# Performance work log

Measured on AMD Instinct MI355X. Metric: run time of the kernel, lower is better.

The kernel has to match this reference:

```python
import jax, jax.numpy as jnp
import numpy as np

N = 100000      # nodes
E = 1600000     # edges per adjacency
NFEAT = 128
NH1 = 128
NH2 = 64
ND1 = 64
P = 100000      # link-prediction pairs


def setup_inputs() -> dict:
    key = jax.random.key(0)
    ks = jax.random.split(key, 20)

    def unif(k, shape, fan):
        s = 1.0 / np.sqrt(fan)
        return jax.random.uniform(k, shape, jnp.float32, -s, s)

    return {
        "x": jax.random.normal(ks[0], (N, NFEAT), jnp.float32),
        "o_edges": jax.random.randint(ks[1], (2, E), 0, N, jnp.int32),
        "o_vals": jax.random.uniform(ks[2], (E,), jnp.float32),
        "s_edges": jax.random.randint(ks[3], (2, E), 0, N, jnp.int32),
        "s_vals": jax.random.uniform(ks[4], (E,), jnp.float32),
        "idx": jax.random.randint(ks[5], (2, P), 0, N, jnp.int64),
        "W_o1": unif(ks[6], (NFEAT, NH1), NFEAT),
        "b_o1": unif(ks[7], (NH1,), NFEAT),
        "W_o2": unif(ks[8], (NH1, NH2), NH1),
        "b_o2": unif(ks[9], (NH2,), NH1),
        "W_s1": unif(ks[10], (NFEAT, NH1), NFEAT),
        "b_s1": unif(ks[11], (NH1,), NFEAT),
        "W_s2": unif(ks[12], (NH1, NH2), NH1),
        "b_s2": unif(ks[13], (NH2,), NH1),
        "ag1": unif(ks[14], (NH2,), NH2),
        "ag2": unif(ks[15], (NH2,), NH2),
        "dec1_W": unif(ks[16], (2 * NH2, ND1), 2 * NH2),
        "dec1_b": unif(ks[17], (ND1,), 2 * NH2),
        "dec2_W": unif(ks[18], (ND1, 1), ND1),
        "dec2_b": unif(ks[19], (1,), ND1),
    }


def _gcn(h, edges, vals, W, b):
    # GraphConvolution: support = h @ W; out = spmm(adj, support) + b
    support = h @ W                                # [N, d_out]
    msg = support[edges[1]] * vals[:, None]        # gather src rows, scale by edge weight
    agg = jax.ops.segment_sum(msg, edges[0], num_segments=N)
    return agg + b


def reference(x, o_edges, o_vals, s_edges, s_vals, idx,
              W_o1, b_o1, W_o2, b_o2, W_s1, b_s1, W_s2, b_s2,
              ag1, ag2, dec1_W, dec1_b, dec2_W, dec2_b):
    # branch 1 (original graph); dropout is identity in eval mode
    x1 = jax.nn.relu(_gcn(x, o_edges, o_vals, W_o1, b_o1))
    x1 = _gcn(x1, o_edges, o_vals, W_o2, b_o2)     # [N, NH2]
    # branch 2 (skip graph)
    x2 = jax.nn.relu(_gcn(x, s_edges, s_vals, W_s1, b_s1))
    x2 = _gcn(x2, s_edges, s_vals, W_s2, b_s2)     # [N, NH2]
    # attention gating: per-node scalar gate broadcast over features
    g = (x1 @ ag1)[:, None] * x1 + (x2 @ ag2)[:, None] * x2  # [N, NH2]
    # gather pair endpoints, concat, MLP decoder (no activation in between)
    feat = jnp.concatenate((g[idx[0]], g[idx[1]]), axis=1)   # [P, 2*NH2]
    o = feat @ dec1_W + dec1_b
    return o @ dec2_W + dec2_b                               # [P, 1]
```

## Files before the change

### kernel.cpp

```cpp
#include <hip/hip_runtime.h>


constexpr int BKT_SHIFT = 8;
constexpr int BKT_NODES = 256;
constexpr int SORT_CAP  = 7168;

typedef __attribute__((ext_vector_type(8))) short bf16x8;
typedef __attribute__((ext_vector_type(4))) float f32x4;

__device__ __forceinline__ float wave_sum64(float x) {
#pragma unroll
    for (int o = 32; o > 0; o >>= 1) x += __shfl_xor(x, o, 64);
    return x;
}

__device__ __forceinline__ unsigned short f2bf(float f) {
    unsigned int u = __float_as_uint(f);
    u += 0x7FFF + ((u >> 16) & 1);
    return (unsigned short)(u >> 16);
}

__device__ __forceinline__ float2 bf2f2(unsigned int u) {
    float2 r;
    r.x = __uint_as_float(u << 16);
    r.y = __uint_as_float(u & 0xFFFF0000u);
    return r;
}


__global__ __launch_bounds__(256) void bhist_k(const int* __restrict__ eo,
                                               const int* __restrict__ es,
                                               int* __restrict__ bcnt,
                                               int E, int N, int nb) {
    __shared__ int lh[1024];
    for (int i = threadIdx.x; i < nb; i += 256) lh[i] = 0;
    __syncthreads();
    int total = 2 * E;
    for (int t = blockIdx.x * 256 + threadIdx.x; t < total; t += gridDim.x * 256) {
        int g = (t >= E) ? 1 : 0;
        int e = g ? t - E : t;
        int dst = (g ? es : eo)[e];
        atomicAdd(&lh[(g * N + dst) >> BKT_SHIFT], 1);
    }
    __syncthreads();
    for (int i = threadIdx.x; i < nb; i += 256) {
        int v = lh[i];
        if (v) atomicAdd(&bcnt[i], v);
    }
}

__global__ __launch_bounds__(1024) void bscan_k(const int* __restrict__ bcnt,
                                                int* __restrict__ bbase,
                                                int* __restrict__ bcur,
                                                int nb, int total) {
    __shared__ int sh[1024];
    int t = threadIdx.x;
    int v = (t < nb) ? bcnt[t] : 0;
    sh[t] = v;
    __syncthreads();
#pragma unroll
    for (int o = 1; o < 1024; o <<= 1) {
        int tv = (t >= o) ? sh[t - o] : 0;
        __syncthreads();
        sh[t] += tv;
        __syncthreads();
    }
    if (t < nb) {
        int b = sh[t] - v;
        bbase[t] = b;
        bcur[t] = b;
    }
    if (t == 0) bbase[nb] = total;
}

__global__ __launch_bounds__(256) void bin_k(const int* __restrict__ eo,
                                             const float* __restrict__ vo,
                                             const int* __restrict__ es,
                                             const float* __restrict__ vs,
                                             int* __restrict__ bcur,
                                             int2* __restrict__ binned,
                                             int E, int N, int nb, int chunk) {
    __shared__ int lcnt[1024];
    __shared__ int lbase[1024];
    int c0 = blockIdx.x * chunk;
    int c1 = min(c0 + chunk, 2 * E);
    for (int i = threadIdx.x; i < nb; i += 256) lcnt[i] = 0;
    __syncthreads();
    for (int t = c0 + threadIdx.x; t < c1; t += 256) {
        int g = (t >= E) ? 1 : 0;
        int e = g ? t - E : t;
        int dst = (g ? es : eo)[e];
        atomicAdd(&lcnt[(g * N + dst) >> BKT_SHIFT], 1);
    }
    __syncthreads();
    for (int i = threadIdx.x; i < nb; i += 256) {
        int v = lcnt[i];
        lbase[i] = v ? atomicAdd(&bcur[i], v) : 0;
        lcnt[i] = 0;
    }
    __syncthreads();
    for (int t = c0 + threadIdx.x; t < c1; t += 256) {
        int g = (t >= E) ? 1 : 0;
        int e = g ? t - E : t;
        const int* edges = g ? es : eo;
        int dst = edges[e];
        int dc = g * N + dst;
        int b = dc >> BKT_SHIFT;
        int pos = lbase[b] + atomicAdd(&lcnt[b], 1);
        int src = edges[E + e];
        float val = (g ? vs : vo)[e];
        binned[pos] = make_int2(((dc & (BKT_NODES - 1)) << 17) | src,
                                __float_as_int(val));
    }
}

__global__ __launch_bounds__(256) void sort_k(const int* __restrict__ bbase,
                                              const int2* __restrict__ binned,
                                              int2* __restrict__ csr,
                                              int* __restrict__ rp2,
                                              int n2, int total) {
    __shared__ int2 lrec[SORT_CAP];
    __shared__ int ldeg[BKT_NODES];
    __shared__ int lsc[BKT_NODES];
    int b = blockIdx.x;
    int base = bbase[b];
    int count = min(bbase[b + 1] - base, SORT_CAP);
    int tid = threadIdx.x;
    for (int k = tid; k < count; k += 256) lrec[k] = binned[base + k];
    ldeg[tid] = 0;
    __syncthreads();
    for (int k = tid; k < count; k += 256) atomicAdd(&ldeg[lrec[k].x >> 17], 1);
    __syncthreads();
    int v = ldeg[tid];
    lsc[tid] = v;
    __syncthreads();
#pragma unroll
    for (int o = 1; o < 256; o <<= 1) {
        int tv = (tid >= o) ? lsc[tid - o] : 0;
        __syncthreads();
        lsc[tid] += tv;
        __syncthreads();
    }
    int excl = lsc[tid] - v;
    int node = b * BKT_NODES + tid;
    if (node < n2) rp2[node] = base + excl;
    if (b == 0 && tid == 0) rp2[n2] = total;
    ldeg[tid] = excl;
    __syncthreads();
    for (int k = tid; k < count; k += 256) {
        int2 r = lrec[k];
        int dl = r.x >> 17;
        int p = atomicAdd(&ldeg[dl], 1);
        csr[base + p] = make_int2(r.x & 0x1FFFF, r.y);
    }
}

__global__ void prep_k(const float* __restrict__ dec1_W, const float* __restrict__ dec1_b,
                       const float* __restrict__ dec2_W, const float* __restrict__ dec2_b,
                       const float* __restrict__ W_o2, const float* __restrict__ b_o2,
                       const float* __restrict__ W_s2, const float* __restrict__ b_s2,
                       const float* __restrict__ ag1, const float* __restrict__ ag2,
                       float* __restrict__ Mo, float* __restrict__ Ms,
                       float* __restrict__ beta, float* __restrict__ cc) {
    __shared__ float vsh[128];
    int t = threadIdx.x;
    float s = 0.f;
    for (int j = 0; j < 64; ++j) s += dec1_W[t * 64 + j] * dec2_W[j];
    vsh[t] = s;
    __syncthreads();
    const float* vlo = vsh;
    const float* vhi = vsh + 64;
    float m0 = 0, m1 = 0, m2 = 0, n0 = 0, n1 = 0, n2 = 0;
    for (int k = 0; k < 64; ++k) {
        float wo = W_o2[t * 64 + k], wsv = W_s2[t * 64 + k];
        m0 += wo * ag1[k];  m1 += wo * vlo[k];  m2 += wo * vhi[k];
        n0 += wsv * ag2[k]; n1 += wsv * vlo[k]; n2 += wsv * vhi[k];
    }
    Mo[0 * 128 + t] = m0; Mo[1 * 128 + t] = m1; Mo[2 * 128 + t] = m2;
    Ms[0 * 128 + t] = n0; Ms[1 * 128 + t] = n1; Ms[2 * 128 + t] = n2;
    if (t == 0) {
        float b0 = 0, b1 = 0, b2 = 0, s0 = 0, s1 = 0, s2 = 0, c0 = 0;
        for (int k = 0; k < 64; ++k) {
            b0 += b_o2[k] * ag1[k]; b1 += b_o2[k] * vlo[k]; b2 += b_o2[k] * vhi[k];
            s0 += b_s2[k] * ag2[k]; s1 += b_s2[k] * vlo[k]; s2 += b_s2[k] * vhi[k];
            c0 += dec1_b[k] * dec2_W[k];
        }
        beta[0] = b0; beta[1] = b1; beta[2] = b2;
        beta[4] = s0; beta[5] = s1; beta[6] = s2;
        *cc = c0 + dec2_b[0];
    }
}

__global__ __launch_bounds__(256) void gemm_mfma2_k(const float* __restrict__ X,
                                                    const float* __restrict__ W0,
                                                    const float* __restrict__ W1,
                                                    unsigned short* __restrict__ S0,
                                                    unsigned short* __restrict__ S1,
                                                    int nrows) {
    __shared__ unsigned short XL[128 * 128];
    __shared__ unsigned short WT[128 * 128];

    const int tid = threadIdx.x;
    const int row0 = blockIdx.x * 128;
    const float4* X4 = (const float4*)X;

#pragma unroll
    for (int i = 0; i < 16; ++i) {
        int f = i * 256 + tid;
        int r = f >> 5, q = f & 31;
        int gr = row0 + r;
        if (gr >= nrows) gr = nrows - 1;
        float4 v = X4[(size_t)gr * 32 + q];
        unsigned int w0 = (unsigned int)f2bf(v.x) | ((unsigned int)f2bf(v.y) << 16);
        unsigned int w1 = (unsigned int)f2bf(v.z) | ((unsigned int)f2bf(v.w) << 16);
        int bp = (q >> 1) ^ (r & 15);
        unsigned int* p = (unsigned int*)&XL[r * 128 + bp * 8 + (q & 1) * 4];
        p[0] = w0;
        p[1] = w1;
    }

    const int w4 = (tid >> 6) * 32;
    const int lr = tid & 15;
    const int kg = (tid >> 4) & 3;

    bf16x8 a[2][4];
    bool a_loaded = false;

    for (int br = 0; br < 2; ++br) {
        const float* W = br ? W1 : W0;
        unsigned short* S = br ? S1 : S0;
        if (br) __syncthreads();
        {
            int c = tid >> 1;
            int kh = (tid & 1) * 64;
#pragma unroll 8
            for (int k2 = 0; k2 < 32; ++k2) {
                int k = kh + 2 * k2;
                unsigned int lo = f2bf(W[k * 128 + c]);
                unsigned int hi = f2bf(W[(k + 1) * 128 + c]);
                int bp = (k >> 3) ^ (c & 15);
                ((unsigned int*)&WT[c * 128 + bp * 8])[(k >> 1) & 3] = lo | (hi << 16);
            }
        }
        __syncthreads();

        if (!a_loaded) {
            a_loaded = true;
#pragma unroll
            for (int rt = 0; rt < 2; ++rt)
#pragma unroll
                for (int kt = 0; kt < 4; ++kt)
                    a[rt][kt] = *(const bf16x8*)&XL[(w4 + rt * 16 + lr) * 128 +
                                                    (((kt * 4 + kg) ^ lr) * 8)];
        }

        f32x4 acc[2][8];
#pragma unroll
        for (int rt = 0; rt < 2; ++rt)
#pragma unroll
            for (int ct = 0; ct < 8; ++ct) acc[rt][ct] = (f32x4){0.f, 0.f, 0.f, 0.f};

#pragma unroll
        for (int ct = 0; ct < 8; ++ct) {
#pragma unroll
            for (int kt = 0; kt < 4; ++kt) {
                bf16x8 b = *(const bf16x8*)&WT[(ct * 16 + lr) * 128 +
                                               (((kt * 4 + kg) ^ lr) * 8)];
                acc[0][ct] = __builtin_amdgcn_mfma_f32_16x16x32_bf16(a[0][kt], b, acc[0][ct], 0, 0, 0);
                acc[1][ct] = __builtin_amdgcn_mfma_f32_16x16x32_bf16(a[1][kt], b, acc[1][ct], 0, 0, 0);
            }
        }

#pragma unroll
        for (int rt = 0; rt < 2; ++rt)
#pragma unroll
            for (int j = 0; j < 4; ++j) {
                int gr = row0 + w4 + rt * 16 + kg * 4 + j;
                if (gr < nrows) {
                    size_t rb = (size_t)gr * 128 + lr;
#pragma unroll
                    for (int ct = 0; ct < 8; ++ct)
                        S[rb + ct * 16] = f2bf(acc[rt][ct][j]);
                }
            }
    }
}

__global__ __launch_bounds__(256) void seg_spmm_fused2_k(
    const int* __restrict__ rp2, const int2* __restrict__ csr,
    const unsigned short* __restrict__ So, const unsigned short* __restrict__ Ss,
    const float* __restrict__ bias_o, const float* __restrict__ bias_s,
    const float* __restrict__ Mo, const float* __restrict__ Ms,
    float4* __restrict__ To, float4* __restrict__ Ts, int n) {
    const int* rp;
    const unsigned int* S;
    const float* bias;
    const float* M;
    float4* T;
    if (blockIdx.y == 0) {
        rp = rp2;     S = (const unsigned int*)So; bias = bias_o; M = Mo; T = To;
    } else {
        rp = rp2 + n; S = (const unsigned int*)Ss; bias = bias_s; M = Ms; T = Ts;
    }
    int wid = (blockIdx.x * 256 + threadIdx.x) >> 6;
    int lane = threadIdx.x & 63;
    if (wid >= n) return;
    int e = rp[wid], end = rp[wid + 1];
    float ax = 0.f, ay = 0.f;
    for (; e + 7 < end; e += 8) {
        int2 c0 = csr[e],     c1 = csr[e + 1], c2 = csr[e + 2], c3 = csr[e + 3];
        int2 c4 = csr[e + 4], c5 = csr[e + 5], c6 = csr[e + 6], c7 = csr[e + 7];
        float2 m0 = bf2f2(S[c0.x * 64 + lane]);
        float2 m1 = bf2f2(S[c1.x * 64 + lane]);
        float2 m2 = bf2f2(S[c2.x * 64 + lane]);
        float2 m3 = bf2f2(S[c3.x * 64 + lane]);
        float2 m4 = bf2f2(S[c4.x * 64 + lane]);
        float2 m5 = bf2f2(S[c5.x * 64 + lane]);
        float2 m6 = bf2f2(S[c6.x * 64 + lane]);
        float2 m7 = bf2f2(S[c7.x * 64 + lane]);
        float v0 = __int_as_float(c0.y), v1 = __int_as_float(c1.y);
        float v2 = __int_as_float(c2.y), v3 = __int_as_float(c3.y);
        float v4 = __int_as_float(c4.y), v5 = __int_as_float(c5.y);
        float v6 = __int_as_float(c6.y), v7 = __int_as_float(c7.y);
        ax += m0.x * v0 + m1.x * v1 + m2.x * v2 + m3.x * v3;
        ay += m0.y * v0 + m1.y * v1 + m2.y * v2 + m3.y * v3;
        ax += m4.x * v4 + m5.x * v5 + m6.x * v6 + m7.x * v7;
        ay += m4.y * v4 + m5.y * v5 + m6.y * v6 + m7.y * v7;
    }
    for (; e + 3 < end; e += 4) {
        int2 c0 = csr[e], c1 = csr[e + 1], c2 = csr[e + 2], c3 = csr[e + 3];
        float2 m0 = bf2f2(S[c0.x * 64 + lane]);
        float2 m1 = bf2f2(S[c1.x * 64 + lane]);
        float2 m2 = bf2f2(S[c2.x * 64 + lane]);
        float2 m3 = bf2f2(S[c3.x * 64 + lane]);
        float v0 = __int_as_float(c0.y), v1 = __int_as_float(c1.y);
        float v2 = __int_as_float(c2.y), v3 = __int_as_float(c3.y);
        ax += m0.x * v0 + m1.x * v1 + m2.x * v2 + m3.x * v3;
        ay += m0.y * v0 + m1.y * v1 + m2.y * v2 + m3.y * v3;
    }
    for (; e < end; ++e) {
        int2 c = csr[e];
        float2 m = bf2f2(S[c.x * 64 + lane]);
        float v = __int_as_float(c.y);
        ax += m.x * v;
        ay += m.y * v;
    }
    float2 bb = ((const float2*)bias)[lane];
    ax = fmaxf(ax + bb.x, 0.f);
    ay = fmaxf(ay + bb.y, 0.f);
    float2 M0 = ((const float2*)(M + 0 * 128))[lane];
    float2 M1 = ((const float2*)(M + 1 * 128))[lane];
    float2 M2 = ((const float2*)(M + 2 * 128))[lane];
    float d = wave_sum64(ax * M0.x + ay * M0.y);
    float u = wave_sum64(ax * M1.x + ay * M1.y);
    float w = wave_sum64(ax * M2.x + ay * M2.y);
    if (lane == 0) T[wid] = make_float4(d, u, w, 0.f);
}

__global__ __launch_bounds__(256) void gate_k(
    const int* __restrict__ rp2, const int2* __restrict__ csr,
    const float4* __restrict__ To, const float4* __restrict__ Ts,
    const float* __restrict__ beta,
    float* __restrict__ a, float* __restrict__ b, int n) {
    int i = blockIdx.x * 256 + threadIdx.x;
    if (i >= n) return;
    float d1 = 0.f, u1 = 0.f, w1 = 0.f;
    {
        int e = rp2[i], end = rp2[i + 1];
        for (; e + 3 < end; e += 4) {
            int2 c0 = csr[e], c1 = csr[e + 1], c2 = csr[e + 2], c3 = csr[e + 3];
            float4 t0 = To[c0.x];
            float4 t1 = To[c1.x];
            float4 t2 = To[c2.x];
            float4 t3 = To[c3.x];
            float v0 = __int_as_float(c0.y), v1 = __int_as_float(c1.y);
            float v2 = __int_as_float(c2.y), v3 = __int_as_float(c3.y);
            d1 += t0.x * v0 + t1.x * v1 + t2.x * v2 + t3.x * v3;
            u1 += t0.y * v0 + t1.y * v1 + t2.y * v2 + t3.y * v3;
            w1 += t0.z * v0 + t1.z * v1 + t2.z * v2 + t3.z * v3;
        }
        for (; e < end; ++e) {
            int2 c = csr[e];
            float4 t = To[c.x];
            float v = __int_as_float(c.y);
            d1 += t.x * v; u1 += t.y * v; w1 += t.z * v;
        }
    }
    float d2 = 0.f, u2 = 0.f, w2 = 0.f;
    {
        int e = rp2[n + i], end = rp2[n + i + 1];
        for (; e + 3 < end; e += 4) {
            int2 c0 = csr[e], c1 = csr[e + 1], c2 = csr[e + 2], c3 = csr[e + 3];
            float4 t0 = Ts[c0.x];
            float4 t1 = Ts[c1.x];
            float4 t2 = Ts[c2.x];
            float4 t3 = Ts[c3.x];
            float v0 = __int_as_float(c0.y), v1 = __int_as_float(c1.y);
            float v2 = __int_as_float(c2.y), v3 = __int_as_float(c3.y);
            d2 += t0.x * v0 + t1.x * v1 + t2.x * v2 + t3.x * v3;
            u2 += t0.y * v0 + t1.y * v1 + t2.y * v2 + t3.y * v3;
            w2 += t0.z * v0 + t1.z * v1 + t2.z * v2 + t3.z * v3;
        }
        for (; e < end; ++e) {
            int2 c = csr[e];
            float4 t = Ts[c.x];
            float v = __int_as_float(c.y);
            d2 += t.x * v; u2 += t.y * v; w2 += t.z * v;
        }
    }
    d1 += beta[0]; u1 += beta[1]; w1 += beta[2];
    d2 += beta[4]; u2 += beta[5]; w2 += beta[6];
    a[i] = d1 * u1 + d2 * u2;
    b[i] = d1 * w1 + d2 * w2;
}

__global__ __launch_bounds__(256) void decode_k(const int* __restrict__ idx,
                                                const float* __restrict__ a,
                                                const float* __restrict__ b,
                                                const float* __restrict__ c,
                                                float* __restrict__ out, int P) {
    int i = blockIdx.x * 256 + threadIdx.x;
    if (i >= P) return;
    out[i] = a[idx[i]] + b[idx[P + i]] + *c;
}


extern "C" void kernel_launch(void* const* d_in, const int* in_sizes, int n_in,
                              void* d_out, int out_size, void* d_ws, size_t ws_size,
                              hipStream_t stream) {
    const float* x      = (const float*)d_in[0];
    const int*   o_edges= (const int*)d_in[1];
    const float* o_vals = (const float*)d_in[2];
    const int*   s_edges= (const int*)d_in[3];
    const float* s_vals = (const float*)d_in[4];
    const int*   idx    = (const int*)d_in[5];
    const float* W_o1   = (const float*)d_in[6];
    const float* b_o1   = (const float*)d_in[7];
    const float* W_o2   = (const float*)d_in[8];
    const float* b_o2   = (const float*)d_in[9];
    const float* W_s1   = (const float*)d_in[10];
    const float* b_s1   = (const float*)d_in[11];
    const float* W_s2   = (const float*)d_in[12];
    const float* b_s2   = (const float*)d_in[13];
    const float* ag1    = (const float*)d_in[14];
    const float* ag2    = (const float*)d_in[15];
    const float* dec1_W = (const float*)d_in[16];
    const float* dec1_b = (const float*)d_in[17];
    const float* dec2_W = (const float*)d_in[18];
    const float* dec2_b = (const float*)d_in[19];
    float* out = (float*)d_out;

    const int N = in_sizes[0] / 128;
    const int E = in_sizes[1] / 2;
    const int P = out_size;
    const int n2 = 2 * N;
    const int nb = (n2 + BKT_NODES - 1) / BKT_NODES;

    const size_t NBH = (size_t)N * 128 * 2;

    char* ws = (char*)d_ws;
    size_t off = 0;
    auto alloc = [&](size_t bytes) {
        char* p = ws + off;
        off += (bytes + 255) & ~(size_t)255;
        return p;
    };

    unsigned short* B0 = (unsigned short*)alloc(NBH);
    unsigned short* B1 = (unsigned short*)alloc(NBH);
    float4* To = (float4*)alloc((size_t)N * 16);
    float4* Ts = (float4*)alloc((size_t)N * 16);
    float* av = (float*)alloc((size_t)P * 4);
    float* bv = (float*)alloc((size_t)P * 4);
    float* Mo = (float*)alloc(3 * 128 * 4);
    float* Ms = (float*)alloc(3 * 128 * 4);
    float* beta = (float*)alloc(32);
    float* cc = (float*)alloc(16);
    int* bcnt  = (int*)alloc((size_t)nb * 4);
    int* bbase = (int*)alloc((size_t)(nb + 1) * 4);
    int* bcur  = (int*)alloc((size_t)nb * 4);
    int* rp2   = (int*)alloc((size_t)(n2 + 1) * 4);
    int2* binned = (int2*)alloc((size_t)2 * E * 8);
    int2* csr    = (int2*)alloc((size_t)2 * E * 8);

    const int nblk = (N + 255) / 256;

    hipMemsetAsync(bcnt, 0, (size_t)nb * 4, stream);
    bhist_k<<<512, 256, 0, stream>>>(o_edges, s_edges, bcnt, E, N, nb);
    bscan_k<<<1, 1024, 0, stream>>>(bcnt, bbase, bcur, nb, 2 * E);
    const int chunk = 8192;
    bin_k<<<(2 * E + chunk - 1) / chunk, 256, 0, stream>>>(
        o_edges, o_vals, s_edges, s_vals, bcur, binned, E, N, nb, chunk);
    sort_k<<<nb, 256, 0, stream>>>(bbase, binned, csr, rp2, n2, 2 * E);

    prep_k<<<1, 128, 0, stream>>>(dec1_W, dec1_b, dec2_W, dec2_b,
                                  W_o2, b_o2, W_s2, b_s2, ag1, ag2,
                                  Mo, Ms, beta, cc);

    gemm_mfma2_k<<<(N + 127) / 128, 256, 0, stream>>>(x, W_o1, W_s1, B0, B1, N);

    dim3 sgrid((N * 64 + 255) / 256, 2);
    seg_spmm_fused2_k<<<sgrid, 256, 0, stream>>>(rp2, csr, B0, B1, b_o1, b_s1,
                                                 Mo, Ms, To, Ts, N);

    gate_k<<<nblk, 256, 0, stream>>>(rp2, csr, To, Ts, beta, av, bv, N);

    decode_k<<<(P + 255) / 256, 256, 0, stream>>>(idx, av, bv, cc, out, P);
}
```

Baseline: 313.5 us.

## Merge GEMM, edge binning and prep into one role-dispatched kernel

Combines the dense feature GEMM, the edge-binning pass and the tiny weight-prep kernel into a single launch where each block picks a role by block index. The independent GEMM and binning work can then run concurrently on the GPU instead of serialising across separate launches, and two launch boundaries go away. In exchange, every block reserves 64 KB of shared memory, including the binning and prep blocks that need far less, which may reduce occupancy for those roles.

New measurement: 293.7 us (median of 2 runs). 1.07x faster.

```diff
diff --git a/kernel.cpp b/kernel.cpp
--- a/kernel.cpp
+++ b/kernel.cpp
@@ -73,16 +73,18 @@
     if (t == 0) bbase[nb] = total;
 }
 
-__global__ __launch_bounds__(256) void bin_k(const int* __restrict__ eo,
-                                             const float* __restrict__ vo,
-                                             const int* __restrict__ es,
-                                             const float* __restrict__ vs,
-                                             int* __restrict__ bcur,
-                                             int2* __restrict__ binned,
-                                             int E, int N, int nb, int chunk) {
-    __shared__ int lcnt[1024];
-    __shared__ int lbase[1024];
-    int c0 = blockIdx.x * chunk;
+
+__device__ __forceinline__ void bin_role(unsigned char* smem, int bb,
+                                         const int* __restrict__ eo,
+                                         const float* __restrict__ vo,
+                                         const int* __restrict__ es,
+                                         const float* __restrict__ vs,
+                                         int* __restrict__ bcur,
+                                         int2* __restrict__ binned,
+                                         int E, int N, int nb, int chunk) {
+    int* lcnt = (int*)smem;
+    int* lbase = lcnt + 1024;
+    int c0 = bb * chunk;
     int c1 = min(c0 + chunk, 2 * E);
     for (int i = threadIdx.x; i < nb; i += 256) lcnt[i] = 0;
     __syncthreads();
@@ -114,94 +116,18 @@
     }
 }
 
-__global__ __launch_bounds__(256) void sort_k(const int* __restrict__ bbase,
-                                              const int2* __restrict__ binned,
-                                              int2* __restrict__ csr,
-                                              int* __restrict__ rp2,
-                                              int n2, int total) {
-    __shared__ int2 lrec[SORT_CAP];
-    __shared__ int ldeg[BKT_NODES];
-    __shared__ int lsc[BKT_NODES];
-    int b = blockIdx.x;
-    int base = bbase[b];
-    int count = min(bbase[b + 1] - base, SORT_CAP);
-    int tid = threadIdx.x;
-    for (int k = tid; k < count; k += 256) lrec[k] = binned[base + k];
-    ldeg[tid] = 0;
-    __syncthreads();
-    for (int k = tid; k < count; k += 256) atomicAdd(&ldeg[lrec[k].x >> 17], 1);
-    __syncthreads();
-    int v = ldeg[tid];
-    lsc[tid] = v;
-    __syncthreads();
-#pragma unroll
-    for (int o = 1; o < 256; o <<= 1) {
-        int tv = (tid >= o) ? lsc[tid - o] : 0;
-        __syncthreads();
-        lsc[tid] += tv;
-        __syncthreads();
-    }
-    int excl = lsc[tid] - v;
-    int node = b * BKT_NODES + tid;
-    if (node < n2) rp2[node] = base + excl;
-    if (b == 0 && tid == 0) rp2[n2] = total;
-    ldeg[tid] = excl;
-    __syncthreads();
-    for (int k = tid; k < count; k += 256) {
-        int2 r = lrec[k];
-        int dl = r.x >> 17;
-        int p = atomicAdd(&ldeg[dl], 1);
-        csr[base + p] = make_int2(r.x & 0x1FFFF, r.y);
-    }
-}
-
-__global__ void prep_k(const float* __restrict__ dec1_W, const float* __restrict__ dec1_b,
-                       const float* __restrict__ dec2_W, const float* __restrict__ dec2_b,
-                       const float* __restrict__ W_o2, const float* __restrict__ b_o2,
-                       const float* __restrict__ W_s2, const float* __restrict__ b_s2,
-                       const float* __restrict__ ag1, const float* __restrict__ ag2,
-                       float* __restrict__ Mo, float* __restrict__ Ms,
-                       float* __restrict__ beta, float* __restrict__ cc) {
-    __shared__ float vsh[128];
-    int t = threadIdx.x;
-    float s = 0.f;
-    for (int j = 0; j < 64; ++j) s += dec1_W[t * 64 + j] * dec2_W[j];
-    vsh[t] = s;
-    __syncthreads();
-    const float* vlo = vsh;
-    const float* vhi = vsh + 64;
-    float m0 = 0, m1 = 0, m2 = 0, n0 = 0, n1 = 0, n2 = 0;
-    for (int k = 0; k < 64; ++k) {
-        float wo = W_o2[t * 64 + k], wsv = W_s2[t * 64 + k];
-        m0 += wo * ag1[k];  m1 += wo * vlo[k];  m2 += wo * vhi[k];
-        n0 += wsv * ag2[k]; n1 += wsv * vlo[k]; n2 += wsv * vhi[k];
-    }
-    Mo[0 * 128 + t] = m0; Mo[1 * 128 + t] = m1; Mo[2 * 128 + t] = m2;
-    Ms[0 * 128 + t] = n0; Ms[1 * 128 + t] = n1; Ms[2 * 128 + t] = n2;
-    if (t == 0) {
-        float b0 = 0, b1 = 0, b2 = 0, s0 = 0, s1 = 0, s2 = 0, c0 = 0;
-        for (int k = 0; k < 64; ++k) {
-            b0 += b_o2[k] * ag1[k]; b1 += b_o2[k] * vlo[k]; b2 += b_o2[k] * vhi[k];
-            s0 += b_s2[k] * ag2[k]; s1 += b_s2[k] * vlo[k]; s2 += b_s2[k] * vhi[k];
-            c0 += dec1_b[k] * dec2_W[k];
-        }
-        beta[0] = b0; beta[1] = b1; beta[2] = b2;
-        beta[4] = s0; beta[5] = s1; beta[6] = s2;
-        *cc = c0 + dec2_b[0];
-    }
-}
-
-__global__ __launch_bounds__(256) void gemm_mfma2_k(const float* __restrict__ X,
-                                                    const float* __restrict__ W0,
-                                                    const float* __restrict__ W1,
-                                                    unsigned short* __restrict__ S0,
-                                                    unsigned short* __restrict__ S1,
-                                                    int nrows) {
-    __shared__ unsigned short XL[128 * 128];
-    __shared__ unsigned short WT[128 * 128];
+__device__ __forceinline__ void gemm_role(unsigned char* smem, int blk,
+                                          const float* __restrict__ X,
+                                          const float* __restrict__ W0,
+                                          const float* __restrict__ W1,
+                                          unsigned short* __restrict__ S0,
+                                          unsigned short* __restrict__ S1,
+                                          int nrows) {
+    unsigned short* XL = (unsigned short*)smem;
+    unsigned short* WT = XL + 128 * 128;
 
     const int tid = threadIdx.x;
-    const int row0 = blockIdx.x * 128;
+    const int row0 = blk * 128;
     const float4* X4 = (const float4*)X;
 
 #pragma unroll
@@ -283,6 +209,124 @@
                         S[rb + ct * 16] = f2bf(acc[rt][ct][j]);
                 }
             }
+    }
+}
+
+__device__ __forceinline__ void prep_role(unsigned char* smem,
+                                          const float* __restrict__ dec1_W,
+                                          const float* __restrict__ dec1_b,
+                                          const float* __restrict__ dec2_W,
+                                          const float* __restrict__ dec2_b,
+                                          const float* __restrict__ W_o2,
+                                          const float* __restrict__ b_o2,
+                                          const float* __restrict__ W_s2,
+                                          const float* __restrict__ b_s2,
+                                          const float* __restrict__ ag1,
+                                          const float* __restrict__ ag2,
+                                          float* __restrict__ Mo,
+                                          float* __restrict__ Ms,
+                                          float* __restrict__ beta,
+                                          float* __restrict__ cc) {
+    float* vsh = (float*)smem;
+    int t = threadIdx.x;
+    if (t < 128) {
+        float s = 0.f;
+        for (int j = 0; j < 64; ++j) s += dec1_W[t * 64 + j] * dec2_W[j];
+        vsh[t] = s;
+    }
+    __syncthreads();
+    if (t < 128) {
+        const float* vlo = vsh;
+        const float* vhi = vsh + 64;
+        float m0 = 0, m1 = 0, m2 = 0, n0 = 0, n1 = 0, n2 = 0;
+        for (int k = 0; k < 64; ++k) {
+            float wo = W_o2[t * 64 + k], wsv = W_s2[t * 64 + k];
+            m0 += wo * ag1[k];  m1 += wo * vlo[k];  m2 += wo * vhi[k];
+            n0 += wsv * ag2[k]; n1 += wsv * vlo[k]; n2 += wsv * vhi[k];
+        }
+        Mo[0 * 128 + t] = m0; Mo[1 * 128 + t] = m1; Mo[2 * 128 + t] = m2;
+        Ms[0 * 128 + t] = n0; Ms[1 * 128 + t] = n1; Ms[2 * 128 + t] = n2;
+        if (t == 0) {
+            float b0 = 0, b1 = 0, b2 = 0, s0 = 0, s1 = 0, s2 = 0, c0 = 0;
+            for (int k = 0; k < 64; ++k) {
+                b0 += b_o2[k] * ag1[k]; b1 += b_o2[k] * vlo[k]; b2 += b_o2[k] * vhi[k];
+                s0 += b_s2[k] * ag2[k]; s1 += b_s2[k] * vlo[k]; s2 += b_s2[k] * vhi[k];
+                c0 += dec1_b[k] * dec2_W[k];
+            }
+            beta[0] = b0; beta[1] = b1; beta[2] = b2;
+            beta[4] = s0; beta[5] = s1; beta[6] = s2;
+            *cc = c0 + dec2_b[0];
+        }
+    }
+}
+
+__global__ __launch_bounds__(256) void fused_k(
+    int gblocks, int binblocks,
+    const float* __restrict__ X, const float* __restrict__ W0,
+    const float* __restrict__ W1, unsigned short* __restrict__ S0,
+    unsigned short* __restrict__ S1, int nrows,
+    const int* __restrict__ eo, const float* __restrict__ vo,
+    const int* __restrict__ es, const float* __restrict__ vs,
+    int* __restrict__ bcur, int2* __restrict__ binned,
+    int E, int N, int nb, int chunk,
+    const float* __restrict__ dec1_W, const float* __restrict__ dec1_b,
+    const float* __restrict__ dec2_W, const float* __restrict__ dec2_b,
+    const float* __restrict__ W_o2, const float* __restrict__ b_o2,
+    const float* __restrict__ W_s2, const float* __restrict__ b_s2,
+    const float* __restrict__ ag1, const float* __restrict__ ag2,
+    float* __restrict__ Mo, float* __restrict__ Ms,
+    float* __restrict__ beta, float* __restrict__ cc) {
+    __shared__ __align__(16) unsigned char smem[64 * 1024];
+    int bid = blockIdx.x;
+    if (bid < gblocks) {
+        gemm_role(smem, bid, X, W0, W1, S0, S1, nrows);
+    } else if (bid < gblocks + binblocks) {
+        bin_role(smem, bid - gblocks, eo, vo, es, vs, bcur, binned, E, N, nb, chunk);
+    } else {
+        prep_role(smem, dec1_W, dec1_b, dec2_W, dec2_b, W_o2, b_o2, W_s2, b_s2,
+                  ag1, ag2, Mo, Ms, beta, cc);
+    }
+}
+
+
+__global__ __launch_bounds__(256) void sort_k(const int* __restrict__ bbase,
+                                              const int2* __restrict__ binned,
+                                              int2* __restrict__ csr,
+                                              int* __restrict__ rp2,
+                                              int n2, int total) {
+    __shared__ int2 lrec[SORT_CAP];
+    __shared__ int ldeg[BKT_NODES];
+    __shared__ int lsc[BKT_NODES];
+    int b = blockIdx.x;
+    int base = bbase[b];
+    int count = min(bbase[b + 1] - base, SORT_CAP);
+    int tid = threadIdx.x;
+    for (int k = tid; k < count; k += 256) lrec[k] = binned[base + k];
+    ldeg[tid] = 0;
+    __syncthreads();
+    for (int k = tid; k < count; k += 256) atomicAdd(&ldeg[lrec[k].x >> 17], 1);
+    __syncthreads();
+    int v = ldeg[tid];
+    lsc[tid] = v;
+    __syncthreads();
+#pragma unroll
+    for (int o = 1; o < 256; o <<= 1) {
+        int tv = (tid >= o) ? lsc[tid - o] : 0;
+        __syncthreads();
+        lsc[tid] += tv;
+        __syncthreads();
+    }
+    int excl = lsc[tid] - v;
+    int node = b * BKT_NODES + tid;
+    if (node < n2) rp2[node] = base + excl;
+    if (b == 0 && tid == 0) rp2[n2] = total;
+    ldeg[tid] = excl;
+    __syncthreads();
+    for (int k = tid; k < count; k += 256) {
+        int2 r = lrec[k];
+        int dl = r.x >> 17;
+        int p = atomicAdd(&ldeg[dl], 1);
+        csr[base + p] = make_int2(r.x & 0x1FFFF, r.y);
     }
 }
 
@@ -488,16 +532,18 @@
     hipMemsetAsync(bcnt, 0, (size_t)nb * 4, stream);
     bhist_k<<<512, 256, 0, stream>>>(o_edges, s_edges, bcnt, E, N, nb);
     bscan_k<<<1, 1024, 0, stream>>>(bcnt, bbase, bcur, nb, 2 * E);
+
     const int chunk = 8192;
-    bin_k<<<(2 * E + chunk - 1) / chunk, 256, 0, stream>>>(
-        o_edges, o_vals, s_edges, s_vals, bcur, binned, E, N, nb, chunk);
+    const int gblocks = (N + 127) / 128;
+    const int binblocks = (2 * E + chunk - 1) / chunk;
+    fused_k<<<gblocks + binblocks + 1, 256, 0, stream>>>(
+        gblocks, binblocks,
+        x, W_o1, W_s1, B0, B1, N,
+        o_edges, o_vals, s_edges, s_vals, bcur, binned, E, N, nb, chunk,
+        dec1_W, dec1_b, dec2_W, dec2_b, W_o2, b_o2, W_s2, b_s2, ag1, ag2,
+        Mo, Ms, beta, cc);
+
     sort_k<<<nb, 256, 0, stream>>>(bbase, binned, csr, rp2, n2, 2 * E);
-
-    prep_k<<<1, 128, 0, stream>>>(dec1_W, dec1_b, dec2_W, dec2_b,
-                                  W_o2, b_o2, W_s2, b_s2, ag1, ag2,
-                                  Mo, Ms, beta, cc);
-
-    gemm_mfma2_k<<<(N + 127) / 128, 256, 0, stream>>>(x, W_o1, W_s1, B0, B1, N);
 
     dim3 sgrid((N * 64 + 255) / 256, 2);
     seg_spmm_fused2_k<<<sgrid, 256, 0, stream>>>(rp2, csr, B0, B1, b_o1, b_s1,
```
